# Optimization experiments

Measured on AMD Instinct MI355X. Metric: run time of the kernel, lower is better.

Reference implementation:

```python
import jax, jax.numpy as jnp
import numpy as np

THETA = 1.0
V_TH = 1.0       # spikingjelly IFNode default v_threshold
SG_ALPHA = 4.0   # spikingjelly surrogate.Sigmoid default alpha


@jax.custom_vjp
def heaviside(x):
    # spike = 1 if membrane - threshold >= 0
    return (x >= 0).astype(x.dtype)

def _heaviside_fwd(x):
    return (x >= 0).astype(x.dtype), x

def _heaviside_bwd(x, g):
    s = jax.nn.sigmoid(SG_ALPHA * x)
    return (g * SG_ALPHA * s * (1.0 - s),)

heaviside.defvjp(_heaviside_fwd, _heaviside_bwd)


@jax.custom_vjp
def spike_aggregate(spike_out, z_total):
    return spike_out

def _sa_fwd(spike_out, z_total):
    return spike_out, z_total

def _sa_bwd(z_total, g):
    surrogate = (z_total > 0).astype(g.dtype) / THETA
    return (jnp.zeros_like(g), g * surrogate)

spike_aggregate.defvjp(_sa_fwd, _sa_bwd)


def setup_inputs() -> dict:
    key = jax.random.key(0)
    k_x, k_w1, k_b1, k_w2, k_b2 = jax.random.split(key, 5)
    B, D_in, H, D_out = 4096, 784, 800, 10
    x = jax.random.uniform(k_x, (B, D_in), dtype=jnp.float32)
    # nn.Linear-style init: U(-1/sqrt(fan_in), 1/sqrt(fan_in))
    s1 = 1.0 / np.sqrt(D_in)
    s2 = 1.0 / np.sqrt(H)
    W1 = jax.random.uniform(k_w1, (H, D_in), jnp.float32, -s1, s1)
    b1 = jax.random.uniform(k_b1, (H,), jnp.float32, -s1, s1)
    W2 = jax.random.uniform(k_w2, (D_out, H), jnp.float32, -s2, s2)
    b2 = jax.random.uniform(k_b2, (D_out,), jnp.float32, -s2, s2)
    return {"x": x, "W1": W1, "b1": b1, "W2": W2, "b2": b2, "T_sim": 32}


def reference(x, W1, b1, W2, b2, T_sim):
    B = x.shape[0]
    x = x.reshape(B, -1)
    # fixed Bernoulli rate encoding (rand_like(x) < x)
    u = jax.random.uniform(jax.random.key(42), x.shape, dtype=x.dtype)
    x_fixed = (u < x).astype(x.dtype)
    # fc1 input is the same every timestep -> compute once
    cur1 = x_fixed @ W1.T + b1                     # [B, 800]

    def step(carry, _):
        v1, v2, count, z_total = carry
        h1 = v1 + cur1
        spk1 = heaviside(h1 - V_TH)
        v1 = h1 * (1.0 - jax.lax.stop_gradient(spk1))  # hard reset to 0, detach_reset
        cur2 = spk1 @ W2.T + b2                    # [B, 10]
        z_total = z_total + cur2
        h2 = v2 + cur2
        spk2 = heaviside(h2 - V_TH)
        v2 = h2 * (1.0 - jax.lax.stop_gradient(spk2))
        count = count + spk2
        return (v1, v2, count, z_total), None

    H, D_out = W1.shape[0], W2.shape[0]
    init = (jnp.zeros((B, H), x.dtype), jnp.zeros((B, D_out), x.dtype),
            jnp.zeros((B, D_out), x.dtype), jnp.zeros((B, D_out), x.dtype))
    (v1, v2, count, z_total), _ = jax.lax.scan(step, init, None, length=T_sim)
    return spike_aggregate(count, z_total)
```

## Files before the change

### kernel.cpp

```cpp
#include <hip/hip_runtime.h>
#include <stdint.h>

#define B_ROWS 4096
#define D_IN   784
#define H_DIM  800
#define D_OUT  10
#define T_SIM  32
#define N_ELEM (B_ROWS * D_IN)
#define CAP    448

__device__ __forceinline__ void threefry2x32(uint32_t k0, uint32_t k1,
                                             uint32_t& x0, uint32_t& x1) {
  uint32_t ks0 = k0, ks1 = k1, ks2 = k0 ^ k1 ^ 0x1BD11BDAu;
  x0 += ks0; x1 += ks1;
#define TF_RND(r) { x0 += x1; x1 = (x1 << (r)) | (x1 >> (32 - (r))); x1 ^= x0; }
  TF_RND(13) TF_RND(15) TF_RND(26) TF_RND(6)
  x0 += ks1; x1 += ks2 + 1u;
  TF_RND(17) TF_RND(29) TF_RND(16) TF_RND(24)
  x0 += ks2; x1 += ks0 + 2u;
  TF_RND(13) TF_RND(15) TF_RND(26) TF_RND(6)
  x0 += ks0; x1 += ks1 + 3u;
  TF_RND(17) TF_RND(29) TF_RND(16) TF_RND(24)
  x0 += ks1; x1 += ks2 + 4u;
  TF_RND(13) TF_RND(15) TF_RND(26) TF_RND(6)
  x0 += ks2; x1 += ks0 + 5u;
#undef TF_RND
}

__global__ __launch_bounds__(256) void gen_xfixed(const float* __restrict__ x,
                                                  float* __restrict__ xf) {
  int i = blockIdx.x * blockDim.x + threadIdx.x;
  if (i >= N_ELEM) return;
  uint32_t c0 = 0u, c1 = (uint32_t)i;
  threefry2x32(0u, 42u, c0, c1);
  uint32_t bits = c0 ^ c1;
  float u = __uint_as_float((bits >> 9) | 0x3F800000u) - 1.0f;
  xf[i] = (u < x[i]) ? 1.0f : 0.0f;
}

#define BM 64
#define BN 64
#define BK 16

__global__ __launch_bounds__(256) void gemm_masks(const float* __restrict__ xf,
                                                  const float* __restrict__ W1,
                                                  const float* __restrict__ b1,
                                                  uint32_t* __restrict__ mb) {
  __shared__ __align__(16) float As[2][BK][BM + 4];
  __shared__ __align__(16) float Bs[2][BK][BN + 4];
  const int m0 = blockIdx.y * BM;
  const int n0 = blockIdx.x * BN;
  const int t  = threadIdx.x;
  const int tx = t & 15, ty = t >> 4;
  const int sM = t >> 2;
  const int sK = (t & 3) * 4;
  const int hB = n0 + sM;
  const bool bOK = (hB < H_DIM);
  const float* aptr = xf + (size_t)(m0 + sM) * D_IN + sK;
  const float* bptr = W1 + (size_t)(bOK ? hB : 0) * D_IN + sK;

  float4 a4 = *(const float4*)(aptr);
  float4 b4 = *(const float4*)(bptr);
  if (!bOK) { b4.x = b4.y = b4.z = b4.w = 0.0f; }

  As[0][sK + 0][sM] = a4.x; As[0][sK + 1][sM] = a4.y;
  As[0][sK + 2][sM] = a4.z; As[0][sK + 3][sM] = a4.w;
  Bs[0][sK + 0][sM] = b4.x; Bs[0][sK + 1][sM] = b4.y;
  Bs[0][sK + 2][sM] = b4.z; Bs[0][sK + 3][sM] = b4.w;
  __syncthreads();

  float acc[4][4] = {};
  const int NT = D_IN / BK;
#pragma unroll 1
  for (int tt = 0; tt < NT; ++tt) {
    const int cur = tt & 1;
    const bool more = (tt + 1 < NT);
    if (more) {
      a4 = *(const float4*)(aptr + (tt + 1) * BK);
      b4 = *(const float4*)(bptr + (tt + 1) * BK);
      if (!bOK) { b4.x = b4.y = b4.z = b4.w = 0.0f; }
    }
    const float (*Ac)[BM + 4] = As[cur];
    const float (*Bc)[BN + 4] = Bs[cur];
#pragma unroll
    for (int kk = 0; kk < BK; kk++) {
      float4 av = *(const float4*)&Ac[kk][ty * 4];
      float4 bv = *(const float4*)&Bc[kk][tx * 4];
      float a[4] = {av.x, av.y, av.z, av.w};
      float b[4] = {bv.x, bv.y, bv.z, bv.w};
#pragma unroll
      for (int mi = 0; mi < 4; mi++)
#pragma unroll
        for (int ni = 0; ni < 4; ni++)
          acc[mi][ni] = __builtin_fmaf(a[mi], b[ni], acc[mi][ni]);
    }
    if (more) {
      const int nxt = cur ^ 1;
      As[nxt][sK + 0][sM] = a4.x; As[nxt][sK + 1][sM] = a4.y;
      As[nxt][sK + 2][sM] = a4.z; As[nxt][sK + 3][sM] = a4.w;
      Bs[nxt][sK + 0][sM] = b4.x; Bs[nxt][sK + 1][sM] = b4.y;
      Bs[nxt][sK + 2][sM] = b4.z; Bs[nxt][sK + 3][sM] = b4.w;
      __syncthreads();
    }
  }

  const int hOut = n0 + tx * 4;
  if (hOut < H_DIM) {
    float4 bb = *(const float4*)&b1[hOut];
#pragma unroll
    for (int mi = 0; mi < 4; mi++) {
      int m = m0 + ty * 4 + mi;
      float c4[4] = {acc[mi][0] + bb.x, acc[mi][1] + bb.y,
                     acc[mi][2] + bb.z, acc[mi][3] + bb.w};
      uint32_t mk4[4];
#pragma unroll
      for (int ni = 0; ni < 4; ni++) {
        float c = c4[ni];
        float v = 0.0f;
        int p = 0;
#pragma unroll 1
        for (int s = 1; s <= T_SIM; s++) {
          float h1 = v + c;
          if (h1 >= 1.0f) { p = s; break; }
          v = h1;
        }
        uint32_t mk = 0;
        if (p) for (int s = p; s <= T_SIM; s += p) mk |= 1u << (s - 1);
        mk4[ni] = mk;
      }
      *(uint4*)&mb[(size_t)m * H_DIM + hOut] =
          make_uint4(mk4[0], mk4[1], mk4[2], mk4[3]);
    }
  }
}

__global__ __launch_bounds__(320) void snn_scan(const uint32_t* __restrict__ mb,
                                                const float* __restrict__ W2,
                                                const float* __restrict__ b2,
                                                float* __restrict__ out) {
  __shared__ __align__(16) float W2T[H_DIM * D_OUT];
  __shared__ __align__(16) uint2 pkS[2][CAP];
  __shared__ int   lenS[2];
  __shared__ float b2f[D_OUT];
  float* c2s = (float*)&pkS[0][0];
  const int tid  = threadIdx.x;
  const int row0 = blockIdx.x * 2;

  if (tid < D_OUT) b2f[tid] = b2[tid];

  if (tid < 128) {
    const int r = tid >> 6, ln = tid & 63;
    const uint64_t lm = (1ull << ln) - 1ull;
    const uint32_t* mrow = mb + (size_t)(row0 + r) * H_DIM;
    uint32_t mv[13];
#pragma unroll
    for (int ch = 0; ch < 13; ++ch) {
      int h = ch * 64 + ln;
      mv[ch] = (h < H_DIM) ? mrow[h] : 0u;
    }
    int off = 0;
#pragma unroll
    for (int ch = 0; ch < 13; ++ch) {
      bool g = (mv[ch] != 0u);
      uint64_t bal = __ballot(g);
      int pos = off + __popcll(bal & lm);
      if (g && pos < CAP) {
        uint2 pk; pk.x = (uint32_t)((ch * 64 + ln) * 40); pk.y = mv[ch];
        pkS[r][pos] = pk;
      }
      off += __popcll(bal);
    }
    if (off <= CAP) {
      int lp = (off + 63) & ~63;
      int i = off + ln;
      if (i < lp) { pkS[r][i].x = 0u; pkS[r][i].y = 0u; }
    }
    if (ln == 0) lenS[r] = off;
  } else {
    for (int e = tid - 128; e < H_DIM * D_OUT; e += 192) {
      int o = e / H_DIM, h = e - o * H_DIM;
      W2T[h * D_OUT + o] = W2[e];
    }
  }
  __syncthreads();

  float s0 = 0.0f, s1 = 0.0f;
  const int j = tid >> 6;
  const int lane = tid & 63;
  const int t = lane & 31;
  const int r = lane >> 5;
  const bool ovf = (lenS[0] > CAP) || (lenS[1] > CAP);
  {
    if (!ovf) {
      const int Lpad = (lenS[r] + 63) & ~63;
      const uint2* pp = pkS[r];
      const char* wbase = (const char*)W2T + 8 * j;
#pragma unroll 4
      for (int i = 0; i < Lpad; ++i) {
        uint2 pk = pp[i];
        float2 w = *(const float2*)(wbase + pk.x);
        bool g = (pk.y >> t) & 1u;
        s0 += g ? w.x : 0.0f;
        s1 += g ? w.y : 0.0f;
      }
    } else {
      const uint32_t* mrow = mb + (size_t)(row0 + r) * H_DIM;
      const uint32_t vbit = 1u << t;
      for (int h = 0; h < H_DIM; ++h) {
        uint32_t mk = mrow[h];
        float2 w = *(const float2*)&W2T[h * D_OUT + 2 * j];
        s0 += (mk & vbit) ? w.x : 0.0f;
        s1 += (mk & vbit) ? w.y : 0.0f;
      }
    }
  }
  __syncthreads();
  c2s[((r * T_SIM) + t) * D_OUT + 2 * j]     = s0;
  c2s[((r * T_SIM) + t) * D_OUT + 2 * j + 1] = s1;
  __syncthreads();

  if (tid < 2 * D_OUT) {
    const int rr = tid / D_OUT, o = tid % D_OUT;
    const float bb = b2f[o];
    float v = 0.0f; int cnt = 0;
#pragma unroll
    for (int tt = 0; tt < T_SIM; ++tt) {
      float cur2 = c2s[((rr * T_SIM) + tt) * D_OUT + o] + bb;
      float h2 = v + cur2;
      bool spk = (h2 >= 1.0f);
      cnt += spk ? 1 : 0;
      v = spk ? 0.0f : h2;
    }
    out[(size_t)(row0 + rr) * D_OUT + o] = (float)cnt;
  }
}

extern "C" void kernel_launch(void* const* d_in, const int* in_sizes, int n_in,
                              void* d_out, int out_size, void* d_ws, size_t ws_size,
                              hipStream_t stream) {
  const float* x  = (const float*)d_in[0];
  const float* W1 = (const float*)d_in[1];
  const float* b1 = (const float*)d_in[2];
  const float* W2 = (const float*)d_in[3];
  const float* b2 = (const float*)d_in[4];
  float* outp = (float*)d_out;

  float*    xf = (float*)d_ws;
  uint32_t* mbuf = (uint32_t*)(xf + N_ELEM);

  gen_xfixed<<<N_ELEM / 256, 256, 0, stream>>>(x, xf);

  dim3 g1((H_DIM + BN - 1) / BN, B_ROWS / BM);
  gemm_masks<<<g1, 256, 0, stream>>>(xf, W1, b1, mbuf);

  snn_scan<<<B_ROWS / 2, 320, 0, stream>>>(mbuf, W2, b2, outp);
}
```

Measured before the change: 304.4 us.

## Transpose GEMM operands to K-major and stream them directly from global memory

```diff
diff --git a/kernel.cpp b/kernel.cpp
--- a/kernel.cpp
+++ b/kernel.cpp
@@ -27,89 +27,105 @@
 #undef TF_RND
 }
 
-__global__ __launch_bounds__(256) void gen_xfixed(const float* __restrict__ x,
-                                                  float* __restrict__ xf) {
-  int i = blockIdx.x * blockDim.x + threadIdx.x;
-  if (i >= N_ELEM) return;
-  uint32_t c0 = 0u, c1 = (uint32_t)i;
-  threefry2x32(0u, 42u, c0, c1);
-  uint32_t bits = c0 ^ c1;
-  float u = __uint_as_float((bits >> 9) | 0x3F800000u) - 1.0f;
-  xf[i] = (u < x[i]) ? 1.0f : 0.0f;
-}
-
-#define BM 64
-#define BN 64
-#define BK 16
-
-__global__ __launch_bounds__(256) void gemm_masks(const float* __restrict__ xf,
-                                                  const float* __restrict__ W1,
+__global__ __launch_bounds__(256) void gen_xfixed_T(const float* __restrict__ x,
+                                                    float* __restrict__ xfT) {
+  const int m = blockIdx.x * 256 + threadIdx.x;
+  const int kb = blockIdx.y * 16;
+#pragma unroll 1
+  for (int kk = 0; kk < 16; ++kk) {
+    const int k = kb + kk;
+    const int i = m * D_IN + k;
+    uint32_t c0 = 0u, c1 = (uint32_t)i;
+    threefry2x32(0u, 42u, c0, c1);
+    uint32_t bits = c0 ^ c1;
+    float u = __uint_as_float((bits >> 9) | 0x3F800000u) - 1.0f;
+    xfT[(size_t)k * B_ROWS + m] = (u < x[i]) ? 1.0f : 0.0f;
+  }
+}
+
+__global__ __launch_bounds__(256) void transpose_w1(const float* __restrict__ W1,
+                                                    float* __restrict__ W1T) {
+  const int idx = blockIdx.x * 256 + threadIdx.x;
+  if (idx >= D_IN * H_DIM) return;
+  const int k = idx / H_DIM;
+  const int h = idx - k * H_DIM;
+  W1T[idx] = W1[h * D_IN + k];
+}
+
+__global__ __launch_bounds__(256) void gemm_masks(const float* __restrict__ xfT,
+                                                  const float* __restrict__ W1T,
                                                   const float* __restrict__ b1,
                                                   uint32_t* __restrict__ mb) {
-  __shared__ __align__(16) float As[2][BK][BM + 4];
-  __shared__ __align__(16) float Bs[2][BK][BN + 4];
-  const int m0 = blockIdx.y * BM;
-  const int n0 = blockIdx.x * BN;
   const int t  = threadIdx.x;
   const int tx = t & 15, ty = t >> 4;
-  const int sM = t >> 2;
-  const int sK = (t & 3) * 4;
-  const int hB = n0 + sM;
-  const bool bOK = (hB < H_DIM);
-  const float* aptr = xf + (size_t)(m0 + sM) * D_IN + sK;
-  const float* bptr = W1 + (size_t)(bOK ? hB : 0) * D_IN + sK;
-
-  float4 a4 = *(const float4*)(aptr);
-  float4 b4 = *(const float4*)(bptr);
-  if (!bOK) { b4.x = b4.y = b4.z = b4.w = 0.0f; }
-
-  As[0][sK + 0][sM] = a4.x; As[0][sK + 1][sM] = a4.y;
-  As[0][sK + 2][sM] = a4.z; As[0][sK + 3][sM] = a4.w;
-  Bs[0][sK + 0][sM] = b4.x; Bs[0][sK + 1][sM] = b4.y;
-  Bs[0][sK + 2][sM] = b4.z; Bs[0][sK + 3][sM] = b4.w;
-  __syncthreads();
+  const int m0   = blockIdx.y * 64;
+  const int n0   = blockIdx.x * 64;
+  const int mBase = m0 + ty * 4;
+  const int hOut  = n0 + tx * 4;
+  const bool bOK  = (hOut < H_DIM);
+  const float* pA = xfT + mBase;
+  const float* pB = W1T + (bOK ? hOut : 0);
 
   float acc[4][4] = {};
-  const int NT = D_IN / BK;
+
+#define LDG4(d, base) d = *(const float4*)(base)
+#define FMA16(AV, BV)                                            \
+  { acc[0][0] = __builtin_fmaf(AV.x, BV.x, acc[0][0]);           \
+    acc[0][1] = __builtin_fmaf(AV.x, BV.y, acc[0][1]);           \
+    acc[0][2] = __builtin_fmaf(AV.x, BV.z, acc[0][2]);           \
+    acc[0][3] = __builtin_fmaf(AV.x, BV.w, acc[0][3]);           \
+    acc[1][0] = __builtin_fmaf(AV.y, BV.x, acc[1][0]);           \
+    acc[1][1] = __builtin_fmaf(AV.y, BV.y, acc[1][1]);           \
+    acc[1][2] = __builtin_fmaf(AV.y, BV.z, acc[1][2]);           \
+    acc[1][3] = __builtin_fmaf(AV.y, BV.w, acc[1][3]);           \
+    acc[2][0] = __builtin_fmaf(AV.z, BV.x, acc[2][0]);           \
+    acc[2][1] = __builtin_fmaf(AV.z, BV.y, acc[2][1]);           \
+    acc[2][2] = __builtin_fmaf(AV.z, BV.z, acc[2][2]);           \
+    acc[2][3] = __builtin_fmaf(AV.z, BV.w, acc[2][3]);           \
+    acc[3][0] = __builtin_fmaf(AV.w, BV.x, acc[3][0]);           \
+    acc[3][1] = __builtin_fmaf(AV.w, BV.y, acc[3][1]);           \
+    acc[3][2] = __builtin_fmaf(AV.w, BV.z, acc[3][2]);           \
+    acc[3][3] = __builtin_fmaf(AV.w, BV.w, acc[3][3]); }
+
+  float4 ca0, ca1, ca2, ca3, cb0, cb1, cb2, cb3;
+  float4 na0, na1, na2, na3, nb0, nb1, nb2, nb3;
+
+  LDG4(ca0, pA + 0 * B_ROWS);  LDG4(cb0, pB + 0 * H_DIM);
+  LDG4(ca1, pA + 1 * B_ROWS);  LDG4(cb1, pB + 1 * H_DIM);
+  LDG4(ca2, pA + 2 * B_ROWS);  LDG4(cb2, pB + 2 * H_DIM);
+  LDG4(ca3, pA + 3 * B_ROWS);  LDG4(cb3, pB + 3 * H_DIM);
+  const float* qA = pA + 4 * B_ROWS;
+  const float* qB = pB + 4 * H_DIM;
+
+#define PREF(a0, a1, a2, a3, b0, b1, b2, b3)                     \
+  { LDG4(a0, qA + 0 * B_ROWS);  LDG4(b0, qB + 0 * H_DIM);        \
+    LDG4(a1, qA + 1 * B_ROWS);  LDG4(b1, qB + 1 * H_DIM);        \
+    LDG4(a2, qA + 2 * B_ROWS);  LDG4(b2, qB + 2 * H_DIM);        \
+    LDG4(a3, qA + 3 * B_ROWS);  LDG4(b3, qB + 3 * H_DIM);        \
+    qA += 4 * B_ROWS;  qB += 4 * H_DIM; }
+#define FMA4G(a0, a1, a2, a3, b0, b1, b2, b3)                    \
+  { FMA16(a0, b0) FMA16(a1, b1) FMA16(a2, b2) FMA16(a3, b3) }
+
 #pragma unroll 1
-  for (int tt = 0; tt < NT; ++tt) {
-    const int cur = tt & 1;
-    const bool more = (tt + 1 < NT);
-    if (more) {
-      a4 = *(const float4*)(aptr + (tt + 1) * BK);
-      b4 = *(const float4*)(bptr + (tt + 1) * BK);
-      if (!bOK) { b4.x = b4.y = b4.z = b4.w = 0.0f; }
-    }
-    const float (*Ac)[BM + 4] = As[cur];
-    const float (*Bc)[BN + 4] = Bs[cur];
-#pragma unroll
-    for (int kk = 0; kk < BK; kk++) {
-      float4 av = *(const float4*)&Ac[kk][ty * 4];
-      float4 bv = *(const float4*)&Bc[kk][tx * 4];
-      float a[4] = {av.x, av.y, av.z, av.w};
-      float b[4] = {bv.x, bv.y, bv.z, bv.w};
-#pragma unroll
-      for (int mi = 0; mi < 4; mi++)
-#pragma unroll
-        for (int ni = 0; ni < 4; ni++)
-          acc[mi][ni] = __builtin_fmaf(a[mi], b[ni], acc[mi][ni]);
-    }
-    if (more) {
-      const int nxt = cur ^ 1;
-      As[nxt][sK + 0][sM] = a4.x; As[nxt][sK + 1][sM] = a4.y;
-      As[nxt][sK + 2][sM] = a4.z; As[nxt][sK + 3][sM] = a4.w;
-      Bs[nxt][sK + 0][sM] = b4.x; Bs[nxt][sK + 1][sM] = b4.y;
-      Bs[nxt][sK + 2][sM] = b4.z; Bs[nxt][sK + 3][sM] = b4.w;
-      __syncthreads();
-    }
-  }
-
-  const int hOut = n0 + tx * 4;
-  if (hOut < H_DIM) {
+  for (int p = 0; p < 97; ++p) {
+    PREF(na0, na1, na2, na3, nb0, nb1, nb2, nb3);
+    FMA4G(ca0, ca1, ca2, ca3, cb0, cb1, cb2, cb3);
+    PREF(ca0, ca1, ca2, ca3, cb0, cb1, cb2, cb3);
+    FMA4G(na0, na1, na2, na3, nb0, nb1, nb2, nb3);
+  }
+  PREF(na0, na1, na2, na3, nb0, nb1, nb2, nb3);
+  FMA4G(ca0, ca1, ca2, ca3, cb0, cb1, cb2, cb3);
+  FMA4G(na0, na1, na2, na3, nb0, nb1, nb2, nb3);
+#undef PREF
+#undef FMA4G
+#undef FMA16
+#undef LDG4
+
+  if (bOK) {
     float4 bb = *(const float4*)&b1[hOut];
 #pragma unroll
     for (int mi = 0; mi < 4; mi++) {
-      int m = m0 + ty * 4 + mi;
+      int m = mBase + mi;
       float c4[4] = {acc[mi][0] + bb.x, acc[mi][1] + bb.y,
                      acc[mi][2] + bb.z, acc[mi][3] + bb.w};
       uint32_t mk4[4];
@@ -245,13 +261,15 @@
   const float* b2 = (const float*)d_in[4];
   float* outp = (float*)d_out;
 
-  float*    xf = (float*)d_ws;
-  uint32_t* mbuf = (uint32_t*)(xf + N_ELEM);
-
-  gen_xfixed<<<N_ELEM / 256, 256, 0, stream>>>(x, xf);
-
-  dim3 g1((H_DIM + BN - 1) / BN, B_ROWS / BM);
-  gemm_masks<<<g1, 256, 0, stream>>>(xf, W1, b1, mbuf);
+  float*    xfT  = (float*)d_ws;
+  float*    W1T  = xfT + (size_t)D_IN * B_ROWS;
+  uint32_t* mbuf = (uint32_t*)(W1T + (size_t)D_IN * H_DIM);
+
+  gen_xfixed_T<<<dim3(16, 49), 256, 0, stream>>>(x, xfT);
+  transpose_w1<<<(D_IN * H_DIM + 255) / 256, 256, 0, stream>>>(W1, W1T);
+
+  dim3 g1(13, 64);
+  gemm_masks<<<g1, 256, 0, stream>>>(xfT, W1T, b1, mbuf);
 
   snn_scan<<<B_ROWS / 2, 320, 0, stream>>>(mbuf, W2, b2, outp);
 }
```

Measured after the change: 378.9 us. +24.5%, slower.

## Transpose GEMM operands and stage tiles via direct global-to-LDS loads

Applied to the files above, without the earlier changes.

```diff
diff --git a/kernel.cpp b/kernel.cpp
--- a/kernel.cpp
+++ b/kernel.cpp
@@ -27,46 +27,60 @@
 #undef TF_RND
 }
 
-__global__ __launch_bounds__(256) void gen_xfixed(const float* __restrict__ x,
-                                                  float* __restrict__ xf) {
-  int i = blockIdx.x * blockDim.x + threadIdx.x;
-  if (i >= N_ELEM) return;
-  uint32_t c0 = 0u, c1 = (uint32_t)i;
-  threefry2x32(0u, 42u, c0, c1);
-  uint32_t bits = c0 ^ c1;
-  float u = __uint_as_float((bits >> 9) | 0x3F800000u) - 1.0f;
-  xf[i] = (u < x[i]) ? 1.0f : 0.0f;
-}
-
-#define BM 64
-#define BN 64
+__global__ __launch_bounds__(256) void gen_xfixed_T(const float* __restrict__ x,
+                                                    float* __restrict__ xfT) {
+  const int m = blockIdx.x * 256 + threadIdx.x;
+  const int kb = blockIdx.y * 16;
+#pragma unroll 1
+  for (int kk = 0; kk < 16; ++kk) {
+    const int k = kb + kk;
+    const int i = m * D_IN + k;
+    uint32_t c0 = 0u, c1 = (uint32_t)i;
+    threefry2x32(0u, 42u, c0, c1);
+    uint32_t bits = c0 ^ c1;
+    float u = __uint_as_float((bits >> 9) | 0x3F800000u) - 1.0f;
+    xfT[(size_t)k * B_ROWS + m] = (u < x[i]) ? 1.0f : 0.0f;
+  }
+}
+
+__global__ __launch_bounds__(256) void transpose_w1(const float* __restrict__ W1,
+                                                    float* __restrict__ W1T) {
+  const int idx = blockIdx.x * 256 + threadIdx.x;
+  if (idx >= D_IN * H_DIM) return;
+  const int k = idx / H_DIM;
+  const int h = idx - k * H_DIM;
+  W1T[idx] = W1[h * D_IN + k];
+}
+
 #define BK 16
 
-__global__ __launch_bounds__(256) void gemm_masks(const float* __restrict__ xf,
-                                                  const float* __restrict__ W1,
+#define GL2LDS(g, l) __builtin_amdgcn_global_load_lds(                      \
+    (const __attribute__((address_space(1))) void*)(g),                     \
+    (__attribute__((address_space(3))) void*)(l), 16, 0, 0)
+
+__global__ __launch_bounds__(256) void gemm_masks(const float* __restrict__ xfT,
+                                                  const float* __restrict__ W1T,
                                                   const float* __restrict__ b1,
                                                   uint32_t* __restrict__ mb) {
-  __shared__ __align__(16) float As[2][BK][BM + 4];
-  __shared__ __align__(16) float Bs[2][BK][BN + 4];
-  const int m0 = blockIdx.y * BM;
-  const int n0 = blockIdx.x * BN;
+  __shared__ __align__(16) float As[2][BK][64];
+  __shared__ __align__(16) float Bs[2][BK][64];
   const int t  = threadIdx.x;
   const int tx = t & 15, ty = t >> 4;
-  const int sM = t >> 2;
-  const int sK = (t & 3) * 4;
-  const int hB = n0 + sM;
-  const bool bOK = (hB < H_DIM);
-  const float* aptr = xf + (size_t)(m0 + sM) * D_IN + sK;
-  const float* bptr = W1 + (size_t)(bOK ? hB : 0) * D_IN + sK;
-
-  float4 a4 = *(const float4*)(aptr);
-  float4 b4 = *(const float4*)(bptr);
-  if (!bOK) { b4.x = b4.y = b4.z = b4.w = 0.0f; }
-
-  As[0][sK + 0][sM] = a4.x; As[0][sK + 1][sM] = a4.y;
-  As[0][sK + 2][sM] = a4.z; As[0][sK + 3][sM] = a4.w;
-  Bs[0][sK + 0][sM] = b4.x; Bs[0][sK + 1][sM] = b4.y;
-  Bs[0][sK + 2][sM] = b4.z; Bs[0][sK + 3][sM] = b4.w;
+  const int m0 = blockIdx.y * 64;
+  const int n0 = blockIdx.x * 64;
+
+  const int w = t >> 6;
+  const int l = t & 63;
+  const int skk = 4 * w + (l >> 4);
+  const int sm  = (l & 15) * 4;
+  const float* gA = xfT + (size_t)skk * B_ROWS + m0 + sm;
+  const float* gB = W1T + (size_t)skk * H_DIM + n0 + sm;
+
+#define STAGE(buf, tt) {                                                    \
+    GL2LDS(gA + (size_t)(tt) * BK * B_ROWS, &As[buf][4 * w][0]);            \
+    GL2LDS(gB + (size_t)(tt) * BK * H_DIM,  &Bs[buf][4 * w][0]); }
+
+  STAGE(0, 0);
   __syncthreads();
 
   float acc[4][4] = {};
@@ -74,18 +88,11 @@
 #pragma unroll 1
   for (int tt = 0; tt < NT; ++tt) {
     const int cur = tt & 1;
-    const bool more = (tt + 1 < NT);
-    if (more) {
-      a4 = *(const float4*)(aptr + (tt + 1) * BK);
-      b4 = *(const float4*)(bptr + (tt + 1) * BK);
-      if (!bOK) { b4.x = b4.y = b4.z = b4.w = 0.0f; }
-    }
-    const float (*Ac)[BM + 4] = As[cur];
-    const float (*Bc)[BN + 4] = Bs[cur];
+    if (tt + 1 < NT) STAGE(cur ^ 1, tt + 1);
 #pragma unroll
     for (int kk = 0; kk < BK; kk++) {
-      float4 av = *(const float4*)&Ac[kk][ty * 4];
-      float4 bv = *(const float4*)&Bc[kk][tx * 4];
+      float4 av = *(const float4*)&As[cur][kk][ty * 4];
+      float4 bv = *(const float4*)&Bs[cur][kk][tx * 4];
       float a[4] = {av.x, av.y, av.z, av.w};
       float b[4] = {bv.x, bv.y, bv.z, bv.w};
 #pragma unroll
@@ -94,15 +101,9 @@
         for (int ni = 0; ni < 4; ni++)
           acc[mi][ni] = __builtin_fmaf(a[mi], b[ni], acc[mi][ni]);
     }
-    if (more) {
-      const int nxt = cur ^ 1;
-      As[nxt][sK + 0][sM] = a4.x; As[nxt][sK + 1][sM] = a4.y;
-      As[nxt][sK + 2][sM] = a4.z; As[nxt][sK + 3][sM] = a4.w;
-      Bs[nxt][sK + 0][sM] = b4.x; Bs[nxt][sK + 1][sM] = b4.y;
-      Bs[nxt][sK + 2][sM] = b4.z; Bs[nxt][sK + 3][sM] = b4.w;
-      __syncthreads();
-    }
-  }
+    __syncthreads();
+  }
+#undef STAGE
 
   const int hOut = n0 + tx * 4;
   if (hOut < H_DIM) {
@@ -195,7 +196,7 @@
       const int Lpad = (lenS[r] + 63) & ~63;
       const uint2* pp = pkS[r];
       const char* wbase = (const char*)W2T + 8 * j;
-#pragma unroll 4
+#pragma unroll 8
       for (int i = 0; i < Lpad; ++i) {
         uint2 pk = pp[i];
         float2 w = *(const float2*)(wbase + pk.x);
@@ -245,13 +246,15 @@
   const float* b2 = (const float*)d_in[4];
   float* outp = (float*)d_out;
 
-  float*    xf = (float*)d_ws;
-  uint32_t* mbuf = (uint32_t*)(xf + N_ELEM);
-
-  gen_xfixed<<<N_ELEM / 256, 256, 0, stream>>>(x, xf);
-
-  dim3 g1((H_DIM + BN - 1) / BN, B_ROWS / BM);
-  gemm_masks<<<g1, 256, 0, stream>>>(xf, W1, b1, mbuf);
+  float*    xfT  = (float*)d_ws;
+  float*    W1T  = xfT + (size_t)D_IN * B_ROWS;
+  uint32_t* mbuf = (uint32_t*)(W1T + (size_t)D_IN * H_DIM);
+
+  gen_xfixed_T<<<dim3(16, 49), 256, 0, stream>>>(x, xfT);
+  transpose_w1<<<(D_IN * H_DIM + 255) / 256, 256, 0, stream>>>(W1, W1T);
+
+  dim3 g1(13, 64);
+  gemm_masks<<<g1, 256, 0, stream>>>(xfT, W1T, b1, mbuf);
 
   snn_scan<<<B_ROWS / 2, 320, 0, stream>>>(mbuf, W2, b2, outp);
 }
```

Result: faster. 280.1 us (-8.0%).
